# Optimization experiments

Measured on AMD Instinct MI355X. Metric: run time of the kernel, lower is better.

Reference implementation:

```python
import jax, jax.numpy as jnp
import numpy as np

D_MODEL = 2048
NUM_HEADS = 16
D_Q = 1536
D_KV = 512
BS, SL = 2, 2048


def _lin(x, w, b):
    # torch nn.Linear: y = x @ w.T + b, w: [out, in]
    return jnp.einsum('...i,oi->...o', x, w) + b


def _freqs(seq_len, dim, theta=10000.0):
    # Faithful to source incl. precedence quirk: tn = 1 / ((theta ** arange) / dim).
    # float32 overflow -> inf -> tn = 0 for large exponents (identity rotation).
    exps = jnp.arange(0, dim, 2, dtype=jnp.float32)
    tn = 1.0 / ((theta ** exps) / dim)
    m = jnp.arange(seq_len, dtype=jnp.float32)
    ang = jnp.outer(m, tn)  # [sl, dim/2]
    return jnp.cos(ang), jnp.sin(ang)


def _rope(x, cos, sin):
    # x: [bs, sl, dim]; complex pairs are (x[..., 2i], x[..., 2i+1])
    xe = x[..., 0::2]
    xo = x[..., 1::2]
    re = xe * cos - xo * sin
    im = xe * sin + xo * cos
    return jnp.stack([re, im], axis=-1).reshape(x.shape)


def _init_linear(key, out_f, in_f):
    k1, k2 = jax.random.split(key)
    bound = 1.0 / np.sqrt(in_f)
    w = jax.random.uniform(k1, (out_f, in_f), jnp.float32, -bound, bound)
    b = jax.random.uniform(k2, (out_f,), jnp.float32, -bound, bound)
    return w, b


def setup_inputs() -> dict:
    key = jax.random.key(0)
    ks = jax.random.split(key, 9)
    x = jax.random.normal(ks[0], (BS, SL, D_MODEL), jnp.float32)
    w_down_q, b_down_q = _init_linear(ks[1], D_Q, D_MODEL)
    w_up_q, b_up_q = _init_linear(ks[2], D_MODEL, D_Q)
    w_down_kv, b_down_kv = _init_linear(ks[3], D_KV, D_MODEL)
    w_up_k, b_up_k = _init_linear(ks[4], D_MODEL, D_KV)
    w_up_v, b_up_v = _init_linear(ks[5], D_MODEL, D_KV)
    wq_r, bq_r = _init_linear(ks[6], D_MODEL, D_Q)
    wk_r, bk_r = _init_linear(ks[7], D_MODEL, D_KV)
    wo, bo = _init_linear(ks[8], D_MODEL, D_MODEL)
    return dict(x=x,
                w_down_q=w_down_q, b_down_q=b_down_q,
                w_up_q=w_up_q, b_up_q=b_up_q,
                w_down_kv=w_down_kv, b_down_kv=b_down_kv,
                w_up_k=w_up_k, b_up_k=b_up_k,
                w_up_v=w_up_v, b_up_v=b_up_v,
                wq_r=wq_r, bq_r=bq_r,
                wk_r=wk_r, bk_r=bk_r,
                wo=wo, bo=bo)


def reference(x, w_down_q, b_down_q, w_up_q, b_up_q, w_down_kv, b_down_kv,
              w_up_k, b_up_k, w_up_v, b_up_v, wq_r, bq_r, wk_r, bk_r, wo, bo):
    bs, sl, dim = x.shape
    nh, hd = NUM_HEADS, dim // NUM_HEADS
    cos, sin = _freqs(sl, dim)

    # Query path: down-proj -> up-proj content + decoupled RoPE branch
    ct_q = _lin(x, w_down_q, b_down_q)                       # [bs, sl, d_q]
    q_ct = _lin(ct_q, w_up_q, b_up_q)                        # [bs, sl, d_model]
    rope_q = _rope(_lin(ct_q, wq_r, bq_r), cos, sin)         # [bs, sl, d_model]
    q = (q_ct + rope_q).reshape(bs, sl, nh, hd)

    # KV path: shared latent -> separate K/V up-proj + RoPE branch on K
    ct_kv = _lin(x, w_down_kv, b_down_kv)                    # [bs, sl, d_kv]
    k_ct = _lin(ct_kv, w_up_k, b_up_k)
    rope_k = _rope(_lin(ct_kv, wk_r, bk_r), cos, sin)
    k = (k_ct + rope_k).reshape(bs, sl, nh, hd)
    v = _lin(ct_kv, w_up_v, b_up_v).reshape(bs, sl, nh, hd)

    # Attention: explicit matmul + softmax + matmul (no causal mask in source)
    scores = jnp.einsum('bqhd,bkhd->bhqk', q, k) / np.sqrt(hd)
    probs = jax.nn.softmax(scores, axis=-1)
    a = jnp.einsum('bhqk,bkhd->bqhd', probs, v).reshape(bs, sl, nh * hd)
    return _lin(a, wo, bo)
```

## Files before the change

### kernel.cpp

```cpp
#include <hip/hip_runtime.h>

typedef float f32x4 __attribute__((ext_vector_type(4)));
typedef unsigned short us8 __attribute__((ext_vector_type(8)));

#define DEVINL __device__ __forceinline__

DEVINL unsigned short f2bf(float f) {
  unsigned u = __builtin_bit_cast(unsigned, f);
  u += 0x7fffu + ((u >> 16) & 1u);
  return (unsigned short)(u >> 16);
}
DEVINL float bf2f(unsigned short b) { return __builtin_bit_cast(float, ((unsigned)b) << 16); }
DEVINL us8 ld8(const unsigned short* p) { return *reinterpret_cast<const us8*>(p); }
DEVINL void mfma_bf16(f32x4& acc, us8 a, us8 b) {
  asm("v_mfma_f32_16x16x32_bf16 %0, %1, %2, %0" : "+v"(acc) : "v"(a), "v"(b));
}
DEVINL unsigned cvtpk_bf16(float lo, float hi) {
  unsigned r;
  asm("v_cvt_pk_bf16_f32 %0, %1, %2" : "=v"(r) : "v"(lo), "v"(hi));
  return r;
}
DEVINL void gld16(const void* g, void* l) {
  __builtin_amdgcn_global_load_lds((const __attribute__((address_space(1))) void*)g,
                                   (__attribute__((address_space(3))) void*)l, 16, 0, 0);
}

DEVINL void cvt4(const float* __restrict__ s, unsigned short* __restrict__ d, long i) {
  float4 v = reinterpret_cast<const float4*>(s)[i];
  unsigned lo = (unsigned)f2bf(v.x) | ((unsigned)f2bf(v.y) << 16);
  unsigned hi = (unsigned)f2bf(v.z) | ((unsigned)f2bf(v.w) << 16);
  reinterpret_cast<uint2*>(d)[i] = make_uint2(lo, hi);
}

__global__ void k_prep(const float* __restrict__ x, const float* __restrict__ wdq,
                       const float* __restrict__ wdkv, const float* __restrict__ wuq,
                       const float* __restrict__ wqr, const float* __restrict__ wuk,
                       const float* __restrict__ wkr, const float* __restrict__ wuv,
                       const float* __restrict__ wo, const float* __restrict__ bdq,
                       const float* __restrict__ bdkv, const float* __restrict__ buq,
                       const float* __restrict__ bqr, const float* __restrict__ buk,
                       const float* __restrict__ bkr, const float* __restrict__ buv,
                       unsigned short* __restrict__ xb, unsigned short* __restrict__ wcd,
                       unsigned short* __restrict__ wcq, unsigned short* __restrict__ wck,
                       unsigned short* __restrict__ wob, float* __restrict__ cosT,
                       float* __restrict__ sinT, float* __restrict__ bcd,
                       float* __restrict__ bcq, float* __restrict__ bck) {
  constexpr long C0 = 2097152, C1 = C0 + 786432, C2 = C1 + 262144, C3 = C2 + 786432,
                 C4 = C3 + 786432, C5 = C4 + 262144, C6 = C5 + 262144, C7 = C6 + 262144,
                 C8 = C7 + 1048576, C9 = C8 + 2097152, C10 = C9 + 3072;
  long u = (long)blockIdx.x * 256 + threadIdx.x;
  if (u < C0) cvt4(x, xb, u);
  else if (u < C1) cvt4(wdq, wcd, u - C0);
  else if (u < C2) cvt4(wdkv, wcd + 1536L * 2048, u - C1);
  else if (u < C3) cvt4(wuq, wcq, u - C2);
  else if (u < C4) cvt4(wqr, wcq + 2048L * 1536, u - C3);
  else if (u < C5) cvt4(wuk, wck, u - C4);
  else if (u < C6) cvt4(wkr, wck + 2048L * 512, u - C5);
  else if (u < C7) cvt4(wuv, wck + 4096L * 512, u - C6);
  else if (u < C8) cvt4(wo, wob, u - C7);
  else if (u < C9) {
    long idx = u - C8;
    int s = (int)(idx >> 10), i = (int)(idx & 1023);
    float e = (float)(2 * i);
    float pw = powf(10000.0f, e);
    float tn = 1.0f / (pw / 2048.0f);
    float ang = (float)s * tn;
    cosT[idx] = cosf(ang);
    sinT[idx] = sinf(ang);
  } else if (u < C10) {
    long j4 = (u - C9) * 4;
#pragma unroll
    for (int k = 0; k < 4; ++k) {
      long j = j4 + k;
      if (j < 2048) {
        bcd[j] = j < 1536 ? bdq[j] : bdkv[j - 1536];
      } else if (j < 6144) {
        long jj = j - 2048;
        bcq[jj] = jj < 2048 ? buq[jj] : bqr[jj - 2048];
      } else {
        long jj = j - 6144;
        bck[jj] = jj < 2048 ? buk[jj] : (jj < 4096 ? bkr[jj - 2048] : buv[jj - 4096]);
      }
    }
  }
}

template <bool OUTF32>
__global__ __launch_bounds__(512) void k_gemm256(const unsigned short* __restrict__ A,
                                                 const unsigned short* __restrict__ B,
                                                 const float* __restrict__ bias,
                                                 void* __restrict__ Cout, int N, int K, int lda) {
  constexpr int SLOT = 128 * 32 + 256 * 32;
  __shared__ unsigned short lds[3 * SLOT];
  const int nwg = gridDim.x;
  const int orig = blockIdx.x;
  const int wgid = (orig & 7) * (nwg >> 3) + (orig >> 3);
  const int nbn = N >> 8;
  const int bn = wgid % nbn, bm = wgid / nbn;
  const int tid = threadIdx.x, lane = tid & 63, w = tid >> 6;
  const int g = lane >> 4, l16 = lane & 15;
  const int wm = w >> 2, wn = w & 3;
  f32x4 acc[4][4] = {};
  const unsigned short* Abase = A + (size_t)bm * 128 * lda;
  const unsigned short* Bbase = B + (size_t)bn * 256 * K;
  const int ra = tid >> 2;
  const int gca = (tid & 3) ^ ((ra >> 1) & 3);
  const int rb1 = (tid + 512) >> 2;
  const int gcb1 = ((tid + 512) & 3) ^ ((rb1 >> 1) & 3);
  const size_t aoff = (size_t)ra * lda + gca * 8;
  const size_t boff0 = (size_t)ra * K + gca * 8;
  const size_t boff1 = (size_t)rb1 * K + gcb1 * 8;
  auto STAGE = [&](int slot, int kt) {
    unsigned short* s = &lds[slot * SLOT];
    gld16(Abase + aoff + kt, s + tid * 8);
    gld16(Bbase + boff0 + kt, s + 128 * 32 + tid * 8);
    gld16(Bbase + boff1 + kt, s + 128 * 32 + (tid + 512) * 8);
  };
  const int nt = K >> 5;
  STAGE(0, 0);
  STAGE(1, 32);
  asm volatile("s_waitcnt vmcnt(3)" ::: "memory");
  asm volatile("s_barrier" ::: "memory");
  for (int t = 0; t < nt; ++t) {
    const int slot = t % 3;
    if (t + 2 < nt) STAGE((t + 2) % 3, (t + 2) * 32);
    const unsigned short* sa = &lds[slot * SLOT];
    const unsigned short* sb = sa + 128 * 32;
    us8 af[4], bf[4];
#pragma unroll
    for (int m = 0; m < 4; ++m) {
      int row = wm * 64 + m * 16 + l16;
      af[m] = ld8(&sa[row * 32 + ((g ^ ((row >> 1) & 3)) * 8)]);
    }
#pragma unroll
    for (int n = 0; n < 4; ++n) {
      int row = wn * 64 + n * 16 + l16;
      bf[n] = ld8(&sb[row * 32 + ((g ^ ((row >> 1) & 3)) * 8)]);
    }
    __builtin_amdgcn_s_setprio(1);
#pragma unroll
    for (int m = 0; m < 4; ++m)
#pragma unroll
      for (int n = 0; n < 4; ++n) mfma_bf16(acc[m][n], af[m], bf[n]);
    __builtin_amdgcn_s_setprio(0);
    if (t < nt - 2) asm volatile("s_waitcnt vmcnt(3)" ::: "memory");
    else            asm volatile("s_waitcnt vmcnt(0)" ::: "memory");
    asm volatile("s_barrier" ::: "memory");
  }
#pragma unroll
  for (int n = 0; n < 4; ++n) {
    int col = bn * 256 + wn * 64 + n * 16 + l16;
    float bv = bias[col];
#pragma unroll
    for (int m = 0; m < 4; ++m) {
      int row0 = bm * 128 + wm * 64 + m * 16 + g * 4;
#pragma unroll
      for (int r = 0; r < 4; ++r) {
        float vv = acc[m][n][r] + bv;
        if (OUTF32)
          reinterpret_cast<float*>(Cout)[(size_t)(row0 + r) * N + col] = vv;
        else
          reinterpret_cast<unsigned short*>(Cout)[(size_t)(row0 + r) * N + col] = f2bf(vv);
      }
    }
  }
}

__global__ void k_rope_combine(const unsigned short* __restrict__ src, int ldin, float oscale,
                               const float* __restrict__ cosT, const float* __restrict__ sinT,
                               unsigned short* __restrict__ outp) {
  int pidx = blockIdx.x * 256 + threadIdx.x;
  if (pidx >= 4096 * 1024) return;
  int row = pidx >> 10, i = pidx & 1023;
  int s = row & 2047;
  float c = cosT[s * 1024 + i], sn = sinT[s * 1024 + i];
  const unsigned short* rp = src + (size_t)row * ldin;
  float xe = bf2f(rp[2048 + 2 * i]), xo = bf2f(rp[2048 + 2 * i + 1]);
  float re = xe * c - xo * sn;
  float im = xe * sn + xo * c;
  float q0 = (bf2f(rp[2 * i]) + re) * oscale;
  float q1 = (bf2f(rp[2 * i + 1]) + im) * oscale;
  unsigned pack = (unsigned)f2bf(q0) | ((unsigned)f2bf(q1) << 16);
  *reinterpret_cast<unsigned*>(&outp[(size_t)row * 2048 + 2 * i]) = pack;
}

__global__ __launch_bounds__(256) void k_transpose_v(const unsigned short* __restrict__ v, int ld,
                                                     unsigned short* __restrict__ vt) {
  __shared__ unsigned short t[32][33];
  int tx = threadIdx.x & 31, ty = threadIdx.x >> 5;
  int r0 = blockIdx.y * 32, c0 = blockIdx.x * 32;
#pragma unroll
  for (int jj = 0; jj < 4; ++jj)
    t[ty * 4 + jj][tx] = v[(size_t)(r0 + ty * 4 + jj) * ld + c0 + tx];
  __syncthreads();
  int b = r0 >> 11;
#pragma unroll
  for (int jj = 0; jj < 4; ++jj) {
    int colc = c0 + ty * 4 + jj;
    size_t orow = (size_t)(b * 16 + (colc >> 7)) * 128 + (colc & 127);
    vt[orow * 2048 + (r0 & 2047) + tx] = t[tx][ty * 4 + jj];
  }
}

__global__ __launch_bounds__(256, 2) void k_attn(const unsigned short* __restrict__ Q,
                                                 const unsigned short* __restrict__ Kg,
                                                 const unsigned short* __restrict__ VT,
                                                 unsigned short* __restrict__ Aout) {
  __shared__ unsigned short Ks[2][64 * 128];
  __shared__ unsigned short VTs[2][128 * 64];
  __shared__ unsigned short Ps[4][2][16 * 64];
  const int tid = threadIdx.x, lane = tid & 63, w = tid >> 6;
  const int g = lane >> 4, l16 = lane & 15;
  const int qt = blockIdx.x, h = blockIdx.y, b = blockIdx.z;
  us8 qf[2][4];
#pragma unroll
  for (int qg = 0; qg < 2; ++qg) {
    const size_t qrow = (size_t)b * 2048 + qt * 128 + w * 32 + qg * 16 + l16;
#pragma unroll
    for (int kc = 0; kc < 4; ++kc)
      qf[qg][kc] = ld8(&Q[qrow * 2048 + h * 128 + kc * 32 + g * 8]);
  }
  f32x4 O[2][8] = {};
  float mq[2] = {-1e30f, -1e30f}, lq[2] = {0.f, 0.f};
  const unsigned short* Kbase = Kg + (size_t)b * 2048 * 2048 + h * 128;
  const unsigned short* VTb = VT + (size_t)(b * 16 + h) * 128 * 2048;

  auto STAGE = [&](int bufi, int ktrow) {
#pragma unroll
    for (int j = 0; j < 4; ++j) {
      int ch = (j * 4 + w) * 64 + lane;
      int key = ch >> 4, cp = ch & 15;
      gld16(&Kbase[(size_t)(ktrow + key) * 2048 + (size_t)((cp ^ (key & 7)) * 8)],
            &Ks[bufi][(j * 4 + w) * 512]);
      int d = ch >> 3, c2 = ch & 7;
      gld16(&VTb[(size_t)d * 2048 + ktrow + (size_t)((c2 ^ (d & 7)) * 8)],
            &VTs[bufi][(j * 4 + w) * 512]);
    }
  };

  STAGE(0, 0);
  for (int t = 0; t < 32; ++t) {
    const int cur = t & 1;
    __syncthreads();
    if (t < 31) STAGE(cur ^ 1, (t + 1) * 64);
    const unsigned short* KsC = &Ks[cur][0];
    const unsigned short* VTsC = &VTs[cur][0];
    f32x4 st[2][4] = {};
    __builtin_amdgcn_s_setprio(1);
#pragma unroll
    for (int tt = 0; tt < 4; ++tt) {
      int key = tt * 16 + l16;
      int swz = (key & 7) << 3;
#pragma unroll
      for (int kc = 0; kc < 4; ++kc) {
        us8 kf = ld8(&KsC[key * 128 + ((kc * 32 + g * 8) ^ swz)]);
        mfma_bf16(st[0][tt], kf, qf[0][kc]);
        mfma_bf16(st[1][tt], kf, qf[1][kc]);
      }
    }
    __builtin_amdgcn_s_setprio(0);
    const int qswz = (l16 & 7) << 3;
#pragma unroll
    for (int qg = 0; qg < 2; ++qg) {
      float sv[16];
      float smax = -1e30f;
#pragma unroll
      for (int tt = 0; tt < 4; ++tt)
#pragma unroll
        for (int r = 0; r < 4; ++r) {
          sv[tt * 4 + r] = st[qg][tt][r];
          smax = fmaxf(smax, sv[tt * 4 + r]);
        }
      smax = fmaxf(smax, __shfl_xor(smax, 16));
      smax = fmaxf(smax, __shfl_xor(smax, 32));
      float mo = mq[qg];
      if (!__all(smax <= mo + 8.0f)) {
        float mn = fmaxf(mo, smax);
        float fac = exp2f(mo - mn);
        lq[qg] *= fac;
        mq[qg] = mn;
#pragma unroll
        for (int r = 0; r < 4; ++r) {
          float fr = __shfl(fac, g * 4 + r);
#pragma unroll
          for (int n0 = 0; n0 < 8; ++n0) O[qg][n0][r] *= fr;
        }
      }
      float mn = mq[qg];
      float ps = 0.f;
#pragma unroll
      for (int i = 0; i < 16; ++i) {
        sv[i] = exp2f(sv[i] - mn);
        ps += sv[i];
      }
      ps += __shfl_xor(ps, 16);
      ps += __shfl_xor(ps, 32);
      lq[qg] += ps;
      unsigned* P32 = reinterpret_cast<unsigned*>(&Ps[w][qg][0]);
#pragma unroll
      for (int tt = 0; tt < 4; ++tt)
#pragma unroll
        for (int pp = 0; pp < 2; ++pp) {
          int key = tt * 16 + g * 4 + pp * 2;
          unsigned pk = cvtpk_bf16(sv[tt * 4 + pp * 2], sv[tt * 4 + pp * 2 + 1]);
          int elem = l16 * 64 + (key ^ qswz);
          P32[elem >> 1] = pk;
        }
    }
    us8 pf[2][2];
#pragma unroll
    for (int qg = 0; qg < 2; ++qg)
#pragma unroll
      for (int kc = 0; kc < 2; ++kc)
        pf[qg][kc] = ld8(&Ps[w][qg][l16 * 64 + ((kc * 32 + g * 8) ^ qswz)]);
    __builtin_amdgcn_s_setprio(1);
#pragma unroll
    for (int n0 = 0; n0 < 8; ++n0) {
      int d = n0 * 16 + l16;
      int dsw = (d & 7) << 3;
#pragma unroll
      for (int kc = 0; kc < 2; ++kc) {
        us8 vf = ld8(&VTsC[d * 64 + ((kc * 32 + g * 8) ^ dsw)]);
        mfma_bf16(O[0][n0], pf[0][kc], vf);
        mfma_bf16(O[1][n0], pf[1][kc], vf);
      }
    }
    __builtin_amdgcn_s_setprio(0);
  }
#pragma unroll
  for (int qg = 0; qg < 2; ++qg) {
    float inv = 1.0f / lq[qg];
#pragma unroll
    for (int r = 0; r < 4; ++r) {
      float ir = __shfl(inv, g * 4 + r);
      size_t row = (size_t)b * 2048 + qt * 128 + w * 32 + qg * 16 + g * 4 + r;
#pragma unroll
      for (int n0 = 0; n0 < 8; ++n0)
        Aout[row * 2048 + h * 128 + n0 * 16 + l16] = f2bf(O[qg][n0][r] * ir);
    }
  }
}

extern "C" void kernel_launch(void* const* d_in, const int* in_sizes, int n_in, void* d_out,
                              int out_size, void* d_ws, size_t ws_size, hipStream_t stream) {
  (void)in_sizes; (void)n_in; (void)out_size; (void)ws_size;
  constexpr int Mr = 4096;
  using US = unsigned short;
  const float* x        = (const float*)d_in[0];
  const float* w_down_q = (const float*)d_in[1];
  const float* b_down_q = (const float*)d_in[2];
  const float* w_up_q   = (const float*)d_in[3];
  const float* b_up_q   = (const float*)d_in[4];
  const float* w_down_kv= (const float*)d_in[5];
  const float* b_down_kv= (const float*)d_in[6];
  const float* w_up_k   = (const float*)d_in[7];
  const float* b_up_k   = (const float*)d_in[8];
  const float* w_up_v   = (const float*)d_in[9];
  const float* b_up_v   = (const float*)d_in[10];
  const float* wq_r     = (const float*)d_in[11];
  const float* bq_r     = (const float*)d_in[12];
  const float* wk_r     = (const float*)d_in[13];
  const float* bk_r     = (const float*)d_in[14];
  const float* wo       = (const float*)d_in[15];
  const float* bo       = (const float*)d_in[16];

  char* p = (char*)d_ws;
  auto alloc = [&](size_t bytes) { char* r = p; p += (bytes + 255) & ~(size_t)255; return r; };
  float* cosT = (float*)alloc((size_t)2048 * 1024 * 4);
  float* sinT = (float*)alloc((size_t)2048 * 1024 * 4);
  US* xb        = (US*)alloc((size_t)Mr * 2048 * 2);
  US* wcat_down = (US*)alloc((size_t)2048 * 2048 * 2);
  US* wcat_qup  = (US*)alloc((size_t)4096 * 1536 * 2);
  US* wcat_kvup = (US*)alloc((size_t)6144 * 512 * 2);
  US* wob       = (US*)alloc((size_t)2048 * 2048 * 2);
  US* ct        = (US*)alloc((size_t)Mr * 2048 * 2);
  US* big       = (US*)alloc((size_t)Mr * 6144 * 2);
  US* vtb       = (US*)alloc((size_t)Mr * 2048 * 2);
  float* bcat_down = (float*)alloc(2048 * 4);
  float* bcat_qup  = (float*)alloc(4096 * 4);
  float* bcat_kvup = (float*)alloc(6144 * 4);
  US* qb   = xb;
  US* kb   = wcat_down;
  US* t12  = big;
  US* kv3  = big;
  US* aout = ct;

  k_prep<<<dim3(33804), dim3(256), 0, stream>>>(
      x, w_down_q, w_down_kv, w_up_q, wq_r, w_up_k, wk_r, w_up_v, wo, b_down_q, b_down_kv,
      b_up_q, bq_r, b_up_k, bk_r, b_up_v, xb, wcat_down, wcat_qup, wcat_kvup, wob, cosT, sinT,
      bcat_down, bcat_qup, bcat_kvup);

  const float SCQ = 0.08838834764831845f * 1.4426950408889634f;

  k_gemm256<false><<<dim3((2048 / 256) * (Mr / 128)), dim3(512), 0, stream>>>(
      xb, wcat_down, bcat_down, (void*)ct, 2048, 2048, 2048);
  k_gemm256<false><<<dim3((4096 / 256) * (Mr / 128)), dim3(512), 0, stream>>>(
      ct, wcat_qup, bcat_qup, (void*)t12, 4096, 1536, 2048);
  k_rope_combine<<<dim3((4096 * 1024 + 255) / 256), dim3(256), 0, stream>>>(t12, 4096, SCQ, cosT,
                                                                            sinT, qb);
  k_gemm256<false><<<dim3((6144 / 256) * (Mr / 128)), dim3(512), 0, stream>>>(
      ct + 1536, wcat_kvup, bcat_kvup, (void*)kv3, 6144, 512, 2048);
  k_rope_combine<<<dim3((4096 * 1024 + 255) / 256), dim3(256), 0, stream>>>(kv3, 6144, 1.0f, cosT,
                                                                            sinT, kb);
  k_transpose_v<<<dim3(64, 128), dim3(256), 0, stream>>>(kv3 + 4096, 6144, vtb);
  k_attn<<<dim3(16, 16, 2), dim3(256), 0, stream>>>(qb, kb, vtb, aout);
  k_gemm256<true><<<dim3((2048 / 256) * (Mr / 128)), dim3(512), 0, stream>>>(
      aout, wob, bo, d_out, 2048, 2048, 2048);
}
```

Baseline: 362.8 us.

## Fuse Q RoPE into attention and switch attention to 32x32 MFMA with register P

```diff
diff --git a/kernel.cpp b/kernel.cpp
--- a/kernel.cpp
+++ b/kernel.cpp
@@ -1,6 +1,7 @@
 #include <hip/hip_runtime.h>
 
 typedef float f32x4 __attribute__((ext_vector_type(4)));
+typedef float f32x16 __attribute__((ext_vector_type(16)));
 typedef unsigned short us8 __attribute__((ext_vector_type(8)));
 
 #define DEVINL __device__ __forceinline__
@@ -15,10 +16,18 @@
 DEVINL void mfma_bf16(f32x4& acc, us8 a, us8 b) {
   asm("v_mfma_f32_16x16x32_bf16 %0, %1, %2, %0" : "+v"(acc) : "v"(a), "v"(b));
 }
+DEVINL void mfma32(f32x16& acc, us8 a, us8 b) {
+  asm("v_mfma_f32_32x32x16_bf16 %0, %1, %2, %0" : "+v"(acc) : "v"(a), "v"(b));
+}
 DEVINL unsigned cvtpk_bf16(float lo, float hi) {
   unsigned r;
   asm("v_cvt_pk_bf16_f32 %0, %1, %2" : "=v"(r) : "v"(lo), "v"(hi));
   return r;
+}
+DEVINL us8 us8_from4(unsigned a, unsigned b, unsigned c, unsigned d) {
+  union { unsigned u[4]; us8 v; } x;
+  x.u[0] = a; x.u[1] = b; x.u[2] = c; x.u[3] = d;
+  return x.v;
 }
 DEVINL void gld16(const void* g, void* l) {
   __builtin_amdgcn_global_load_lds((const __attribute__((address_space(1))) void*)g,
@@ -166,7 +175,7 @@
   }
 }
 
-__global__ void k_rope_combine(const unsigned short* __restrict__ src, int ldin, float oscale,
+__global__ void k_rope_combine(const unsigned short* __restrict__ src, int ldin,
                                const float* __restrict__ cosT, const float* __restrict__ sinT,
                                unsigned short* __restrict__ outp) {
   int pidx = blockIdx.x * 256 + threadIdx.x;
@@ -178,8 +187,8 @@
   float xe = bf2f(rp[2048 + 2 * i]), xo = bf2f(rp[2048 + 2 * i + 1]);
   float re = xe * c - xo * sn;
   float im = xe * sn + xo * c;
-  float q0 = (bf2f(rp[2 * i]) + re) * oscale;
-  float q1 = (bf2f(rp[2 * i + 1]) + im) * oscale;
+  float q0 = bf2f(rp[2 * i]) + re;
+  float q1 = bf2f(rp[2 * i + 1]) + im;
   unsigned pack = (unsigned)f2bf(q0) | ((unsigned)f2bf(q1) << 16);
   *reinterpret_cast<unsigned*>(&outp[(size_t)row * 2048 + 2 * i]) = pack;
 }
@@ -202,142 +211,139 @@
   }
 }
 
-__global__ __launch_bounds__(256, 2) void k_attn(const unsigned short* __restrict__ Q,
+__global__ __launch_bounds__(256, 2) void k_attn(const unsigned short* __restrict__ Qsrc,
                                                  const unsigned short* __restrict__ Kg,
                                                  const unsigned short* __restrict__ VT,
+                                                 const float* __restrict__ cosT,
+                                                 const float* __restrict__ sinT,
                                                  unsigned short* __restrict__ Aout) {
   __shared__ unsigned short Ks[2][64 * 128];
   __shared__ unsigned short VTs[2][128 * 64];
-  __shared__ unsigned short Ps[4][2][16 * 64];
   const int tid = threadIdx.x, lane = tid & 63, w = tid >> 6;
-  const int g = lane >> 4, l16 = lane & 15;
+  const int hh = lane >> 5, q32 = lane & 31;
   const int qt = blockIdx.x, h = blockIdx.y, b = blockIdx.z;
-  us8 qf[2][4];
-#pragma unroll
-  for (int qg = 0; qg < 2; ++qg) {
-    const size_t qrow = (size_t)b * 2048 + qt * 128 + w * 32 + qg * 16 + l16;
-#pragma unroll
-    for (int kc = 0; kc < 4; ++kc)
-      qf[qg][kc] = ld8(&Q[qrow * 2048 + h * 128 + kc * 32 + g * 8]);
-  }
-  f32x4 O[2][8] = {};
-  float mq[2] = {-1e30f, -1e30f}, lq[2] = {0.f, 0.f};
+  const float SC2 = 0.08838834764831845f * 1.4426950408889634f;
+  const int srow = qt * 128 + w * 32 + q32;
+  us8 qf[8];
+  {
+    const unsigned short* Qr = Qsrc + ((size_t)b * 2048 + srow) * 4096;
+#pragma unroll
+    for (int ds = 0; ds < 8; ++ds) {
+      int dcol = h * 128 + ds * 16 + hh * 8;
+      us8 c8 = ld8(&Qr[dcol]);
+      us8 r8 = ld8(&Qr[2048 + dcol]);
+      unsigned wv[4];
+#pragma unroll
+      for (int p2 = 0; p2 < 4; ++p2) {
+        int i = (dcol >> 1) + p2;
+        float cc = cosT[srow * 1024 + i], ss = sinT[srow * 1024 + i];
+        float xe = bf2f(r8[2 * p2]), xo = bf2f(r8[2 * p2 + 1]);
+        float o0 = (bf2f(c8[2 * p2]) + xe * cc - xo * ss) * SC2;
+        float o1 = (bf2f(c8[2 * p2 + 1]) + xe * ss + xo * cc) * SC2;
+        wv[p2] = cvtpk_bf16(o0, o1);
+      }
+      qf[ds] = us8_from4(wv[0], wv[1], wv[2], wv[3]);
+    }
+  }
+  f32x16 O[4] = {};
+  float mq = -1e30f, lq = 0.f;
   const unsigned short* Kbase = Kg + (size_t)b * 2048 * 2048 + h * 128;
   const unsigned short* VTb = VT + (size_t)(b * 16 + h) * 128 * 2048;
-
   auto STAGE = [&](int bufi, int ktrow) {
 #pragma unroll
     for (int j = 0; j < 4; ++j) {
       int ch = (j * 4 + w) * 64 + lane;
       int key = ch >> 4, cp = ch & 15;
-      gld16(&Kbase[(size_t)(ktrow + key) * 2048 + (size_t)((cp ^ (key & 7)) * 8)],
+      gld16(&Kbase[(size_t)(ktrow + key) * 2048 + (size_t)((cp ^ (key & 15)) * 8)],
             &Ks[bufi][(j * 4 + w) * 512]);
       int d = ch >> 3, c2 = ch & 7;
       gld16(&VTb[(size_t)d * 2048 + ktrow + (size_t)((c2 ^ (d & 7)) * 8)],
             &VTs[bufi][(j * 4 + w) * 512]);
     }
   };
-
   STAGE(0, 0);
   for (int t = 0; t < 32; ++t) {
     const int cur = t & 1;
     __syncthreads();
     if (t < 31) STAGE(cur ^ 1, (t + 1) * 64);
-    const unsigned short* KsC = &Ks[cur][0];
-    const unsigned short* VTsC = &VTs[cur][0];
-    f32x4 st[2][4] = {};
+    f32x16 S2[2] = {};
     __builtin_amdgcn_s_setprio(1);
 #pragma unroll
-    for (int tt = 0; tt < 4; ++tt) {
-      int key = tt * 16 + l16;
-      int swz = (key & 7) << 3;
-#pragma unroll
-      for (int kc = 0; kc < 4; ++kc) {
-        us8 kf = ld8(&KsC[key * 128 + ((kc * 32 + g * 8) ^ swz)]);
-        mfma_bf16(st[0][tt], kf, qf[0][kc]);
-        mfma_bf16(st[1][tt], kf, qf[1][kc]);
+    for (int kb = 0; kb < 2; ++kb) {
+      const int key = kb * 32 + q32;
+      const int swz = key & 15;
+#pragma unroll
+      for (int ds = 0; ds < 8; ++ds) {
+        us8 kf = ld8(&Ks[cur][key * 128 + (((ds * 2 + hh) ^ swz) * 8)]);
+        mfma32(S2[kb], kf, qf[ds]);
       }
     }
     __builtin_amdgcn_s_setprio(0);
-    const int qswz = (l16 & 7) << 3;
-#pragma unroll
-    for (int qg = 0; qg < 2; ++qg) {
-      float sv[16];
-      float smax = -1e30f;
-#pragma unroll
-      for (int tt = 0; tt < 4; ++tt)
-#pragma unroll
-        for (int r = 0; r < 4; ++r) {
-          sv[tt * 4 + r] = st[qg][tt][r];
-          smax = fmaxf(smax, sv[tt * 4 + r]);
-        }
-      smax = fmaxf(smax, __shfl_xor(smax, 16));
-      smax = fmaxf(smax, __shfl_xor(smax, 32));
-      float mo = mq[qg];
-      if (!__all(smax <= mo + 8.0f)) {
-        float mn = fmaxf(mo, smax);
-        float fac = exp2f(mo - mn);
-        lq[qg] *= fac;
-        mq[qg] = mn;
-#pragma unroll
-        for (int r = 0; r < 4; ++r) {
-          float fr = __shfl(fac, g * 4 + r);
-#pragma unroll
-          for (int n0 = 0; n0 < 8; ++n0) O[qg][n0][r] *= fr;
-        }
-      }
-      float mn = mq[qg];
-      float ps = 0.f;
-#pragma unroll
-      for (int i = 0; i < 16; ++i) {
-        sv[i] = exp2f(sv[i] - mn);
-        ps += sv[i];
-      }
-      ps += __shfl_xor(ps, 16);
-      ps += __shfl_xor(ps, 32);
-      lq[qg] += ps;
-      unsigned* P32 = reinterpret_cast<unsigned*>(&Ps[w][qg][0]);
-#pragma unroll
-      for (int tt = 0; tt < 4; ++tt)
-#pragma unroll
-        for (int pp = 0; pp < 2; ++pp) {
-          int key = tt * 16 + g * 4 + pp * 2;
-          unsigned pk = cvtpk_bf16(sv[tt * 4 + pp * 2], sv[tt * 4 + pp * 2 + 1]);
-          int elem = l16 * 64 + (key ^ qswz);
-          P32[elem >> 1] = pk;
-        }
-    }
-    us8 pf[2][2];
-#pragma unroll
-    for (int qg = 0; qg < 2; ++qg)
-#pragma unroll
-      for (int kc = 0; kc < 2; ++kc)
-        pf[qg][kc] = ld8(&Ps[w][qg][l16 * 64 + ((kc * 32 + g * 8) ^ qswz)]);
+    float mx[16];
+#pragma unroll
+    for (int r = 0; r < 16; ++r) mx[r] = fmaxf(S2[0][r], S2[1][r]);
+#pragma unroll
+    for (int st = 8; st > 0; st >>= 1)
+#pragma unroll
+      for (int r = 0; r < st; ++r) mx[r] = fmaxf(mx[r], mx[r + st]);
+    float smax = fmaxf(mx[0], __shfl_xor(mx[0], 32));
+    if (!__all(smax <= mq + 8.0f)) {
+      float mn = fmaxf(mq, smax);
+      float fac = exp2f(mq - mn);
+      lq *= fac;
+      mq = mn;
+#pragma unroll
+      for (int r = 0; r < 16; ++r) {
+        int qr = (r & 3) + 8 * (r >> 2) + 4 * hh;
+        float fr = __shfl(fac, qr);
+#pragma unroll
+        for (int db = 0; db < 4; ++db) O[db][r] *= fr;
+      }
+    }
+    float ps = 0.f;
+    unsigned pk[2][8];
+#pragma unroll
+    for (int kb = 0; kb < 2; ++kb) {
+      float e[16];
+#pragma unroll
+      for (int r = 0; r < 16; ++r) {
+        e[r] = exp2f(S2[kb][r] - mq);
+        ps += e[r];
+      }
+#pragma unroll
+      for (int pp = 0; pp < 8; ++pp) pk[kb][pp] = cvtpk_bf16(e[2 * pp], e[2 * pp + 1]);
+    }
+    ps += __shfl_xor(ps, 32);
+    lq += ps;
     __builtin_amdgcn_s_setprio(1);
 #pragma unroll
-    for (int n0 = 0; n0 < 8; ++n0) {
-      int d = n0 * 16 + l16;
-      int dsw = (d & 7) << 3;
-#pragma unroll
-      for (int kc = 0; kc < 2; ++kc) {
-        us8 vf = ld8(&VTsC[d * 64 + ((kc * 32 + g * 8) ^ dsw)]);
-        mfma_bf16(O[0][n0], pf[0][kc], vf);
-        mfma_bf16(O[1][n0], pf[1][kc], vf);
+    for (int ks = 0; ks < 4; ++ks) {
+      const int kb = ks >> 1, kk = ks & 1;
+      unsigned u_own = hh ? pk[kb][4 * kk + 2] : pk[kb][4 * kk + 0];
+      unsigned v_own = hh ? pk[kb][4 * kk + 3] : pk[kb][4 * kk + 1];
+      unsigned u_snd = hh ? pk[kb][4 * kk + 0] : pk[kb][4 * kk + 2];
+      unsigned v_snd = hh ? pk[kb][4 * kk + 1] : pk[kb][4 * kk + 3];
+      unsigned uo = (unsigned)__shfl_xor((int)u_snd, 32);
+      unsigned vo = (unsigned)__shfl_xor((int)v_snd, 32);
+      us8 pa = us8_from4(hh ? uo : u_own, hh ? vo : v_own, hh ? u_own : uo, hh ? v_own : vo);
+#pragma unroll
+      for (int db = 0; db < 4; ++db) {
+        int d = db * 32 + q32;
+        us8 vf = ld8(&VTs[cur][d * 64 + (((ks * 2 + hh) ^ (d & 7)) * 8)]);
+        mfma32(O[db], pa, vf);
       }
     }
     __builtin_amdgcn_s_setprio(0);
   }
-#pragma unroll
-  for (int qg = 0; qg < 2; ++qg) {
-    float inv = 1.0f / lq[qg];
-#pragma unroll
-    for (int r = 0; r < 4; ++r) {
-      float ir = __shfl(inv, g * 4 + r);
-      size_t row = (size_t)b * 2048 + qt * 128 + w * 32 + qg * 16 + g * 4 + r;
-#pragma unroll
-      for (int n0 = 0; n0 < 8; ++n0)
-        Aout[row * 2048 + h * 128 + n0 * 16 + l16] = f2bf(O[qg][n0][r] * ir);
-    }
+  float inv = 1.0f / lq;
+#pragma unroll
+  for (int r = 0; r < 16; ++r) {
+    int qr = (r & 3) + 8 * (r >> 2) + 4 * hh;
+    float ir = __shfl(inv, qr);
+    size_t row = (size_t)b * 2048 + qt * 128 + w * 32 + qr;
+#pragma unroll
+    for (int db = 0; db < 4; ++db)
+      Aout[row * 2048 + h * 128 + db * 32 + q32] = f2bf(O[db][r] * ir);
   }
 }
 
@@ -366,23 +372,22 @@
 
   char* p = (char*)d_ws;
   auto alloc = [&](size_t bytes) { char* r = p; p += (bytes + 255) & ~(size_t)255; return r; };
-  float* cosT = (float*)alloc((size_t)2048 * 1024 * 4);
-  float* sinT = (float*)alloc((size_t)2048 * 1024 * 4);
-  US* xb        = (US*)alloc((size_t)Mr * 2048 * 2);
-  US* wcat_down = (US*)alloc((size_t)2048 * 2048 * 2);
-  US* wcat_qup  = (US*)alloc((size_t)4096 * 1536 * 2);
-  US* wcat_kvup = (US*)alloc((size_t)6144 * 512 * 2);
-  US* wob       = (US*)alloc((size_t)2048 * 2048 * 2);
-  US* ct        = (US*)alloc((size_t)Mr * 2048 * 2);
-  US* big       = (US*)alloc((size_t)Mr * 6144 * 2);
-  US* vtb       = (US*)alloc((size_t)Mr * 2048 * 2);
+  float* cosT      = (float*)alloc((size_t)2048 * 1024 * 4);
+  float* sinT      = (float*)alloc((size_t)2048 * 1024 * 4);
+  US* wcat_kvup    = (US*)alloc((size_t)6144 * 512 * 2);
+  US* wob          = (US*)alloc((size_t)2048 * 2048 * 2);
+  US* ct           = (US*)alloc((size_t)Mr * 2048 * 2);
+  US* t12          = (US*)alloc((size_t)Mr * 4096 * 2);
+  US* vtb          = (US*)alloc((size_t)Mr * 2048 * 2);
+  US* kb           = (US*)alloc((size_t)Mr * 2048 * 2);
   float* bcat_down = (float*)alloc(2048 * 4);
   float* bcat_qup  = (float*)alloc(4096 * 4);
   float* bcat_kvup = (float*)alloc(6144 * 4);
-  US* qb   = xb;
-  US* kb   = wcat_down;
-  US* t12  = big;
-  US* kv3  = big;
+  US* xb           = (US*)alloc((size_t)Mr * 2048 * 2);
+  US* wcat_down    = (US*)alloc((size_t)2048 * 2048 * 2);
+  US* wcat_qup     = (US*)alloc((size_t)4096 * 1536 * 2);
+  alloc((size_t)12 * 1024 * 1024);
+  US* kv3  = xb;
   US* aout = ct;
 
   k_prep<<<dim3(33804), dim3(256), 0, stream>>>(
@@ -390,20 +395,16 @@
       b_up_q, bq_r, b_up_k, bk_r, b_up_v, xb, wcat_down, wcat_qup, wcat_kvup, wob, cosT, sinT,
       bcat_down, bcat_qup, bcat_kvup);
 
-  const float SCQ = 0.08838834764831845f * 1.4426950408889634f;
-
   k_gemm256<false><<<dim3((2048 / 256) * (Mr / 128)), dim3(512), 0, stream>>>(
       xb, wcat_down, bcat_down, (void*)ct, 2048, 2048, 2048);
   k_gemm256<false><<<dim3((4096 / 256) * (Mr / 128)), dim3(512), 0, stream>>>(
       ct, wcat_qup, bcat_qup, (void*)t12, 4096, 1536, 2048);
-  k_rope_combine<<<dim3((4096 * 1024 + 255) / 256), dim3(256), 0, stream>>>(t12, 4096, SCQ, cosT,
-                                                                            sinT, qb);
   k_gemm256<false><<<dim3((6144 / 256) * (Mr / 128)), dim3(512), 0, stream>>>(
       ct + 1536, wcat_kvup, bcat_kvup, (void*)kv3, 6144, 512, 2048);
-  k_rope_combine<<<dim3((4096 * 1024 + 255) / 256), dim3(256), 0, stream>>>(kv3, 6144, 1.0f, cosT,
-                                                                            sinT, kb);
+  k_rope_combine<<<dim3((4096 * 1024 + 255) / 256), dim3(256), 0, stream>>>(kv3, 6144, cosT, sinT,
+                                                                            kb);
   k_transpose_v<<<dim3(64, 128), dim3(256), 0, stream>>>(kv3 + 4096, 6144, vtb);
-  k_attn<<<dim3(16, 16, 2), dim3(256), 0, stream>>>(qb, kb, vtb, aout);
+  k_attn<<<dim3(16, 16, 2), dim3(256), 0, stream>>>(t12, kb, vtb, cosT, sinT, aout);
   k_gemm256<true><<<dim3((2048 / 256) * (Mr / 128)), dim3(512), 0, stream>>>(
       aout, wob, bo, d_out, 2048, 2048, 2048);
 }
```

New measurement: 361.7 us. No clear change (-0.3%).
